# Optimization experiments

Hardware: AMD Instinct MI355X
Metric: run time of the kernel (lower is better)

Reference implementation:

```python
import jax, jax.numpy as jnp
import numpy as np

INPUT_DIM = 512
NUM_CLASSES = 1000


def setup_inputs() -> dict:
    key = jax.random.key(0)
    kx, kw, kb = jax.random.split(key, 3)
    x = jax.random.normal(kx, (16384, INPUT_DIM), dtype=jnp.float32)
    # Stacked per-class Linear(input_dim, 2) params: W [C, 2, D], b [C, 2]
    lim = 1.0 / np.sqrt(INPUT_DIM)
    W = jax.random.uniform(kw, (NUM_CLASSES, 2, INPUT_DIM), dtype=jnp.float32, minval=-lim, maxval=lim)
    b = jax.random.uniform(kb, (NUM_CLASSES, 2), dtype=jnp.float32, minval=-lim, maxval=lim)
    return {"x": x, "W": W, "b": b}


def reference(x, W, b):
    # logits[b, c, t] = x[b, :] @ W[c, t, :] + b[c, t]
    logits = jnp.einsum("bd,ctd->bct", x, W) + b[None, :, :]  # [B, C, 2]
    # LogSoftmax over the 2 logits per class (torch dim=1 of the [B,2] slice)
    return jax.nn.log_softmax(logits, axis=-1)
```

## Files before the change

### kernel.cpp

```cpp
#include <hip/hip_runtime.h>
#include <cstdint>
#include <cstddef>

typedef unsigned short u16;
typedef unsigned int u32;
typedef __bf16 bf16x8 __attribute__((ext_vector_type(8)));
typedef float f32x4 __attribute__((ext_vector_type(4)));

#define M_TOT 16384
#define C_TOT 1000
#define N_PAD 1024
#define K_TOT 512
#define OUT_STRIDE 2000
#define BM 128
#define BN 128
#define BK 32
#define KSTEPS (K_TOT / BK)

__device__ __forceinline__ u16 f2bf(float f) {
  u32 u = __float_as_uint(f);
  u = (u + 0x7FFFu + ((u >> 16) & 1u)) >> 16;
  return (u16)u;
}

__global__ __launch_bounds__(256) void cvt_kernel(const float* __restrict__ src,
                                                  u16* __restrict__ dst, int n8) {
  int i = blockIdx.x * blockDim.x + threadIdx.x;
  if (i >= n8) return;
  const float4* s = (const float4*)src;
  float4 a = s[2 * i], b = s[2 * i + 1];
  ushort4 r0, r1;
  r0.x = f2bf(a.x); r0.y = f2bf(a.y); r0.z = f2bf(a.z); r0.w = f2bf(a.w);
  r1.x = f2bf(b.x); r1.y = f2bf(b.y); r1.z = f2bf(b.z); r1.w = f2bf(b.w);
  ushort4* d = (ushort4*)dst;
  d[2 * i] = r0;
  d[2 * i + 1] = r1;
}

__global__ __launch_bounds__(256) void wdiff_kernel(const float* __restrict__ W,
                                                    const float* __restrict__ b,
                                                    u16* __restrict__ wd,
                                                    float* __restrict__ bd) {
  const int i = blockIdx.x * blockDim.x + threadIdx.x;
  const int c = i >> 6;
  const int seg = i & 63;
  if (c >= N_PAD) return;
  ushort4 r0 = {0, 0, 0, 0}, r1 = {0, 0, 0, 0};
  if (c < C_TOT) {
    const float4* w0 = (const float4*)(W + (size_t)(2 * c) * K_TOT) + seg * 2;
    const float4* w1 = (const float4*)(W + (size_t)(2 * c + 1) * K_TOT) + seg * 2;
    float4 a0 = w0[0], a1 = w0[1], c0 = w1[0], c1 = w1[1];
    r0.x = f2bf(a0.x - c0.x); r0.y = f2bf(a0.y - c0.y);
    r0.z = f2bf(a0.z - c0.z); r0.w = f2bf(a0.w - c0.w);
    r1.x = f2bf(a1.x - c1.x); r1.y = f2bf(a1.y - c1.y);
    r1.z = f2bf(a1.z - c1.z); r1.w = f2bf(a1.w - c1.w);
    if (seg == 0) bd[c] = b[2 * c] - b[2 * c + 1];
  } else if (seg == 0) {
    bd[c] = 0.0f;
  }
  ushort4* d = (ushort4*)(wd + (size_t)c * K_TOT);
  d[seg * 2] = r0;
  d[seg * 2 + 1] = r1;
}

__device__ __forceinline__ void gload_lds(const u16* g, u16* l) {
  __builtin_amdgcn_global_load_lds((const __attribute__((address_space(1))) u32*)g,
                                   (__attribute__((address_space(3))) u32*)l, 16, 0, 0);
}

__global__ __launch_bounds__(256, 2) void gemm_ls_kernel(const u16* __restrict__ A,
                                                         const u16* __restrict__ B,
                                                         const float* __restrict__ bdiff,
                                                         float* __restrict__ out) {
  __shared__ u16 As[2][BM * BK];
  __shared__ u16 Bs[2][BN * BK];

  const int tid = threadIdx.x;
  const int lane = tid & 63;
  const int w = tid >> 6;
  const int wm = w >> 1;
  const int wn = w & 1;
  const int m0 = blockIdx.y * BM;
  const int n0 = blockIdx.x * BN;

  const int off0 = tid * 16;
  const int off1 = off0 + 4096;
  const int r0 = off0 >> 6, c0e = (off0 & 63) >> 1;
  const int r1 = off1 >> 6, c1e = (off1 & 63) >> 1;

  const u16* gA0 = A + (size_t)(m0 + r0) * K_TOT + c0e;
  const u16* gA1 = A + (size_t)(m0 + r1) * K_TOT + c1e;
  const u16* gB0 = B + (size_t)(n0 + r0) * K_TOT + c0e;
  const u16* gB1 = B + (size_t)(n0 + r1) * K_TOT + c1e;

  u16* lA0[2] = { &As[0][off0 >> 1], &As[1][off0 >> 1] };
  u16* lA1[2] = { &As[0][off1 >> 1], &As[1][off1 >> 1] };
  u16* lB0[2] = { &Bs[0][off0 >> 1], &Bs[1][off0 >> 1] };
  u16* lB1[2] = { &Bs[0][off1 >> 1], &Bs[1][off1 >> 1] };

  f32x4 acc[4][4] = {};

  gload_lds(gA0, lA0[0]);
  gload_lds(gA1, lA1[0]);
  gload_lds(gB0, lB0[0]);
  gload_lds(gB1, lB1[0]);
  __syncthreads();

  const int ar = lane & 15;
  const int kq = (lane >> 4) * 16;

  int cur = 0;
  for (int kt = 0; kt < KSTEPS; ++kt) {
    if (kt < KSTEPS - 1) {
      const int ko = (kt + 1) * BK;
      const int nb = cur ^ 1;
      gload_lds(gA0 + ko, lA0[nb]);
      gload_lds(gA1 + ko, lA1[nb]);
      gload_lds(gB0 + ko, lB0[nb]);
      gload_lds(gB1 + ko, lB1[nb]);
    }

    bf16x8 af[4], bf[4];
#pragma unroll
    for (int mi = 0; mi < 4; ++mi) {
      const int row = wm * 64 + mi * 16 + ar;
      af[mi] = *(const bf16x8*)((const char*)&As[cur][0] + row * 64 + kq);
    }
#pragma unroll
    for (int ni = 0; ni < 4; ++ni) {
      const int row = wn * 64 + ni * 16 + ar;
      bf[ni] = *(const bf16x8*)((const char*)&Bs[cur][0] + row * 64 + kq);
    }
#pragma unroll
    for (int mi = 0; mi < 4; ++mi)
#pragma unroll
      for (int ni = 0; ni < 4; ++ni)
        acc[mi][ni] = __builtin_amdgcn_mfma_f32_16x16x32_bf16(af[mi], bf[ni], acc[mi][ni], 0, 0, 0);

    __syncthreads();
    cur ^= 1;
  }

  float bd_r[4];
  int ncol[4];
#pragma unroll
  for (int ni = 0; ni < 4; ++ni) {
    const int n = n0 + wn * 64 + ni * 16 + ar;
    ncol[ni] = n;
    bd_r[ni] = bdiff[n];
  }
  const int rbase = m0 + wm * 64 + (lane >> 4) * 4;

#pragma unroll
  for (int mi = 0; mi < 4; ++mi) {
#pragma unroll
    for (int ni = 0; ni < 4; ++ni) {
      if (ncol[ni] < C_TOT) {
#pragma unroll
        for (int j = 0; j < 4; ++j) {
          const float d = acc[mi][ni][j] + bd_r[ni];
          const float o0 = fminf(d, 0.0f) - __logf(1.0f + __expf(-fabsf(d)));
          const int row = rbase + mi * 16 + j;
          float2 v;
          v.x = o0;
          v.y = o0 - d;
          *(float2*)(out + (size_t)row * OUT_STRIDE + 2 * ncol[ni]) = v;
        }
      }
    }
  }
}

__global__ __launch_bounds__(256) void naive_kernel(const float* __restrict__ x,
                                                    const float* __restrict__ W,
                                                    const float* __restrict__ b,
                                                    float* __restrict__ out) {
  __shared__ float xs[K_TOT];
  const int row = blockIdx.x;
  for (int i = threadIdx.x; i < K_TOT; i += 256) xs[i] = x[(size_t)row * K_TOT + i];
  __syncthreads();
  for (int c = threadIdx.x; c < C_TOT; c += 256) {
    const float* w0 = W + (size_t)c * 1024;
    float l0 = b[c * 2], l1 = b[c * 2 + 1];
    for (int k = 0; k < K_TOT; ++k) {
      const float xv = xs[k];
      l0 += xv * w0[k];
      l1 += xv * w0[K_TOT + k];
    }
    const float d = l0 - l1;
    const float t = __logf(1.0f + __expf(-fabsf(d)));
    out[(size_t)row * OUT_STRIDE + c * 2]     = fminf(d, 0.0f) - t;
    out[(size_t)row * OUT_STRIDE + c * 2 + 1] = fminf(-d, 0.0f) - t;
  }
}

extern "C" void kernel_launch(void* const* d_in, const int* in_sizes, int n_in,
                              void* d_out, int out_size, void* d_ws, size_t ws_size,
                              hipStream_t stream) {
  const float* x = (const float*)d_in[0];
  const float* W = (const float*)d_in[1];
  const float* b = (const float*)d_in[2];
  float* out = (float*)d_out;

  const size_t nx = (size_t)M_TOT * K_TOT;
  const size_t nwd = (size_t)N_PAD * K_TOT;
  const size_t need = (nx + nwd) * sizeof(u16) + N_PAD * sizeof(float);

  if (ws_size < need) {
    naive_kernel<<<M_TOT, 256, 0, stream>>>(x, W, b, out);
    return;
  }

  u16* xb = (u16*)d_ws;
  u16* wd = xb + nx;
  float* bd = (float*)(wd + nwd);

  cvt_kernel<<<(int)(nx / 8 + 255) / 256, 256, 0, stream>>>(x, xb, (int)(nx / 8));
  wdiff_kernel<<<(N_PAD * 64) / 256, 256, 0, stream>>>(W, b, wd, bd);

  dim3 grid(N_PAD / BN, M_TOT / BM);
  gemm_ls_kernel<<<grid, 256, 0, stream>>>(xb, wd, bd, out);
}
```

Before: 58.67 us.

## Remap GEMM workgroups across XCDs, raise occupancy, use nontemporal output stores

Switches to a 1D grid and remaps block IDs so that consecutive blocks on the same XCD (interleaved by bid&7) cover contiguous M/N tiles, aiming for better L2 reuse of A and B per chiplet. Launch bounds go from 2 to 3 waves per SIMD to raise occupancy. The epilogue is reordered by column with a whole-tile fast path, and output stores become nontemporal to avoid polluting the caches with the large 131MB output. Higher occupancy may force register pressure or spills with 64 accumulator floats.

```diff
diff --git a/kernel.cpp b/kernel.cpp
--- a/kernel.cpp
+++ b/kernel.cpp
@@ -6,6 +6,7 @@
 typedef unsigned int u32;
 typedef __bf16 bf16x8 __attribute__((ext_vector_type(8)));
 typedef float f32x4 __attribute__((ext_vector_type(4)));
+typedef float f32x2 __attribute__((ext_vector_type(2)));
 
 #define M_TOT 16384
 #define C_TOT 1000
@@ -16,6 +17,9 @@
 #define BN 128
 #define BK 32
 #define KSTEPS (K_TOT / BK)
+#define MTILES (M_TOT / BM)
+#define NTILES (N_PAD / BN)
+#define NWG (MTILES * NTILES)
 
 __device__ __forceinline__ u16 f2bf(float f) {
   u32 u = __float_as_uint(f);
@@ -68,7 +72,7 @@
                                    (__attribute__((address_space(3))) u32*)l, 16, 0, 0);
 }
 
-__global__ __launch_bounds__(256, 2) void gemm_ls_kernel(const u16* __restrict__ A,
+__global__ __launch_bounds__(256, 3) void gemm_ls_kernel(const u16* __restrict__ A,
                                                          const u16* __restrict__ B,
                                                          const float* __restrict__ bdiff,
                                                          float* __restrict__ out) {
@@ -80,8 +84,11 @@
   const int w = tid >> 6;
   const int wm = w >> 1;
   const int wn = w & 1;
-  const int m0 = blockIdx.y * BM;
-  const int n0 = blockIdx.x * BN;
+
+  const int bid = blockIdx.x;
+  const int wg = (bid & 7) * (NWG / 8) + (bid >> 3);
+  const int m0 = (wg >> 3) * BM;
+  const int n0 = (wg & 7) * BN;
 
   const int off0 = tid * 16;
   const int off1 = off0 + 4096;
@@ -141,30 +148,25 @@
     cur ^= 1;
   }
 
-  float bd_r[4];
-  int ncol[4];
+  const int rbase = m0 + wm * 64 + (lane >> 4) * 4;
+  const bool full = (n0 + BN <= C_TOT);
+
 #pragma unroll
   for (int ni = 0; ni < 4; ++ni) {
     const int n = n0 + wn * 64 + ni * 16 + ar;
-    ncol[ni] = n;
-    bd_r[ni] = bdiff[n];
-  }
-  const int rbase = m0 + wm * 64 + (lane >> 4) * 4;
-
-#pragma unroll
-  for (int mi = 0; mi < 4; ++mi) {
-#pragma unroll
-    for (int ni = 0; ni < 4; ++ni) {
-      if (ncol[ni] < C_TOT) {
+    if (full || n < C_TOT) {
+      const float bd_r = bdiff[n];
+#pragma unroll
+      for (int mi = 0; mi < 4; ++mi) {
 #pragma unroll
         for (int j = 0; j < 4; ++j) {
-          const float d = acc[mi][ni][j] + bd_r[ni];
+          const float d = acc[mi][ni][j] + bd_r;
           const float o0 = fminf(d, 0.0f) - __logf(1.0f + __expf(-fabsf(d)));
           const int row = rbase + mi * 16 + j;
-          float2 v;
+          f32x2 v;
           v.x = o0;
           v.y = o0 - d;
-          *(float2*)(out + (size_t)row * OUT_STRIDE + 2 * ncol[ni]) = v;
+          __builtin_nontemporal_store(v, (f32x2*)(out + (size_t)row * OUT_STRIDE + 2 * n));
         }
       }
     }
@@ -218,6 +220,5 @@
   cvt_kernel<<<(int)(nx / 8 + 255) / 256, 256, 0, stream>>>(x, xb, (int)(nx / 8));
   wdiff_kernel<<<(N_PAD * 64) / 256, 256, 0, stream>>>(W, b, wd, bd);
 
-  dim3 grid(N_PAD / BN, M_TOT / BM);
-  gemm_ls_kernel<<<grid, 256, 0, stream>>>(xb, wd, bd, out);
-}
+  gemm_ls_kernel<<<NWG, 256, 0, stream>>>(xb, wd, bd, out);
+}
```

After: 61.21 us. 4.3% more time.
